# Kernel tuning notes

Hardware: AMD Instinct MI355X
Metric: run time of the kernel (lower is better)

Reference implementation:

```python
import jax, jax.numpy as jnp
import numpy as np

B, T, E, H, D = 2, 2048, 1024, 16, 64
SCALE = 1.0 / float(np.sqrt(D))


def setup_inputs() -> dict:
    key = jax.random.key(0)
    ks = jax.random.split(key, 8)
    n = lambda k, sh, s=1.0: jax.random.normal(k, sh, dtype=jnp.float32) * s
    # torch nn.Linear weights are [out_features, in_features]; xavier-ish scale
    return {
        "query": n(ks[0], (B, T, E)),
        "key_": n(ks[1], (B, T, E)),
        "value": n(ks[2], (B, T, E)),
        "attn_mask": n(ks[3], (T, T), 0.1),
        "Wq": n(ks[4], (H * D, E), 1.0 / float(np.sqrt(E))),
        "Wk": n(ks[5], (H * D, E), 1.0 / float(np.sqrt(E))),
        "Wv": n(ks[6], (H * D, E), 1.0 / float(np.sqrt(E))),
        "Wo": n(ks[7], (E, H * D), 1.0 / float(np.sqrt(H * D))),
    }


def reference(query, key_, value, attn_mask, Wq, Wk, Wv, Wo):
    # projections (no bias), reshape to [B, T, H, D]
    Q = (query @ Wq.T).reshape(B, T, H, D)
    K = (key_ @ Wk.T).reshape(B, -1, H, D)
    V = (value @ Wv.T).reshape(B, -1, H, D)
    # scores [B, T, H, S]; additive [T, S] mask broadcast over B and H
    score = jnp.einsum("bthd,bshd->bths", Q, K) * SCALE
    score = score + attn_mask[:, None, :]
    prob = jax.nn.softmax(score, axis=-1)  # dropout is identity in eval mode
    attn = jnp.einsum("bths,bshd->bthd", prob, V)  # [B, T, H, D]
    x = attn.reshape(B, T, H * D) @ Wo.T  # output projection
    return x
```

## Files before the change

kernel.cpp:

```cpp
#include <hip/hip_runtime.h>


typedef __attribute__((ext_vector_type(8))) short s8v;
typedef __attribute__((ext_vector_type(4))) float f4v;

typedef __attribute__((address_space(1))) const void* gas_t;
typedef __attribute__((address_space(3))) void* las_t;

#define GLOAD_LDS(src, dst) \
  __builtin_amdgcn_global_load_lds((gas_t)(src), (las_t)(dst), 16, 0, 0)
#define MFMA16(a, b, c) __builtin_amdgcn_mfma_f32_16x16x32_bf16((a), (b), (c), 0, 0, 0)

#if __has_builtin(__builtin_amdgcn_exp2f)
#define EXP2(x) __builtin_amdgcn_exp2f(x)
#else
#define EXP2(x) exp2f(x)
#endif

static constexpr int Bn = 2, Tn = 2048, En = 1024, Hn = 16, Dn = 64;
static constexpr float kScale = 0.125f;
static constexpr float kLog2e = 1.4426950408889634f;

union P8 { s8v v; unsigned short u[8]; };

__device__ __forceinline__ unsigned short f2bf(float f) {
  unsigned int x = __float_as_uint(f);
  x += 0x7fffu + ((x >> 16) & 1u);
  return (unsigned short)(x >> 16);
}

__device__ __forceinline__ int cvtpk(float lo, float hi) {
  int r;
  asm("v_cvt_pk_bf16_f32 %0, %1, %2" : "=v"(r) : "v"(lo), "v"(hi));
  return r;
}

__device__ __forceinline__ void cast8(const float* __restrict__ src, int j,
                                      unsigned short* __restrict__ out, int i) {
  float4 a = ((const float4*)src)[2 * j];
  float4 b = ((const float4*)src)[2 * j + 1];
  P8 p;
  p.u[0] = f2bf(a.x); p.u[1] = f2bf(a.y); p.u[2] = f2bf(a.z); p.u[3] = f2bf(a.w);
  p.u[4] = f2bf(b.x); p.u[5] = f2bf(b.y); p.u[6] = f2bf(b.z); p.u[7] = f2bf(b.w);
  ((s8v*)out)[i] = p.v;
}

__global__ void cast3_kernel(const float* __restrict__ a, const float* __restrict__ b,
                             const float* __restrict__ c,
                             unsigned short* __restrict__ out, int n8) {
  int i = blockIdx.x * blockDim.x + threadIdx.x;
  const int stride = gridDim.x * blockDim.x;
  const int total = 3 * n8;
  for (; i < total; i += stride) {
    const float* src = (i < n8) ? a : (i < 2 * n8) ? b : c;
    const int j = (i < n8) ? i : (i < 2 * n8) ? i - n8 : i - 2 * n8;
    cast8(src, j, out, i);
  }
}

__global__ void cast4_kernel(const float* __restrict__ a, const float* __restrict__ b,
                             const float* __restrict__ c, const float* __restrict__ d,
                             unsigned short* __restrict__ out, int n8) {
  int i = blockIdx.x * blockDim.x + threadIdx.x;
  const int stride = gridDim.x * blockDim.x;
  const int total = 4 * n8;
  for (; i < total; i += stride) {
    const int which = i / n8;
    const float* src = (which == 0) ? a : (which == 1) ? b : (which == 2) ? c : d;
    cast8(src, i - which * n8, out, i);
  }
}

__global__ __launch_bounds__(64) void maskpack_kernel(const float* __restrict__ mask,
                                                      unsigned int* __restrict__ mPB) {
  __shared__ float tile[16][65];
  const int qt = blockIdx.x, st = blockIdx.y;
  const int tid = threadIdx.x;
#pragma unroll
  for (int i = 0; i < 16; ++i)
    tile[i][tid] = mask[(size_t)(qt * 16 + i) * Tn + st * 64 + tid];
  __syncthreads();
  const int lr = tid & 15, lg = tid >> 4;
  float o[16];
#pragma unroll
  for (int n = 0; n < 4; ++n)
#pragma unroll
    for (int rg = 0; rg < 4; ++rg)
      o[n * 4 + rg] = tile[lr][n * 16 + lg * 4 + rg] * kLog2e;
  unsigned int wds[8];
#pragma unroll
  for (int i = 0; i < 8; ++i)
    wds[i] = ((unsigned int)f2bf(o[2 * i + 1]) << 16) | f2bf(o[2 * i]);
  uint4* dst = (uint4*)(mPB + ((size_t)(qt * 32 + st) * 64 + tid) * 8);
  dst[0] = make_uint4(wds[0], wds[1], wds[2], wds[3]);
  dst[1] = make_uint4(wds[4], wds[5], wds[6], wds[7]);
}

__global__ __launch_bounds__(256) void gemm3_kernel(
    const unsigned short* __restrict__ qx, const unsigned short* __restrict__ kx,
    const unsigned short* __restrict__ vxa, const unsigned short* __restrict__ wqx,
    const unsigned short* __restrict__ wkx, const unsigned short* __restrict__ wvx,
    unsigned short* __restrict__ Qh, unsigned short* __restrict__ Kh,
    unsigned short* __restrict__ Vtg) {
  constexpr int K = 1024;
  __shared__ unsigned short As[128 * 64];
  __shared__ unsigned short Bs[128 * 64];
  const int tid = threadIdx.x;
  const int w = tid >> 6, l = tid & 63;
  const int wr = w >> 1, wc = w & 1;
  const int lr = l & 15, lg = l >> 4;

  const int id0 = blockIdx.x;
  const int rid = (id0 & 7) * 96 + (id0 >> 3);
  const int z = rid >> 8;
  const int t8 = rid & 255;
  const int m0 = (z < 2) ? (t8 >> 3) * 128 : (t8 & 7) * 128;
  const int n0 = (z < 2) ? (t8 & 7) * 128 : (t8 >> 3) * 128;

  const unsigned short* A = (z == 0) ? qx : (z == 1) ? kx : wvx;
  const unsigned short* W = (z == 0) ? wqx : (z == 1) ? wkx : vxa;

  f4v acc[4][4] = {};

  for (int k0 = 0; k0 < K; k0 += 64) {
#pragma unroll
    for (int jj = 0; jj < 4; ++jj) {
      const int q = jj * 256 + tid;
      const int r = q >> 3, c = q & 7;
      const int cs = c ^ (r & 7);
      GLOAD_LDS(A + (size_t)(m0 + r) * K + k0 + cs * 8,
                (char*)As + (jj * 256 + w * 64) * 16);
      GLOAD_LDS(W + (size_t)(n0 + r) * K + k0 + cs * 8,
                (char*)Bs + (jj * 256 + w * 64) * 16);
    }
    __syncthreads();
#pragma unroll
    for (int kk = 0; kk < 2; ++kk) {
      s8v af[4], bf[4];
      const int kc = kk * 4 + lg;
#pragma unroll
      for (int i = 0; i < 4; ++i) {
        const int ra = wr * 64 + i * 16 + lr;
        const int rb = wc * 64 + i * 16 + lr;
        af[i] = *(const s8v*)((const char*)As + ra * 128 + ((kc ^ (ra & 7)) << 4));
        bf[i] = *(const s8v*)((const char*)Bs + rb * 128 + ((kc ^ (rb & 7)) << 4));
      }
#pragma unroll
      for (int mi = 0; mi < 4; ++mi)
#pragma unroll
        for (int nj = 0; nj < 4; ++nj)
          acc[mi][nj] = MFMA16(af[mi], bf[nj], acc[mi][nj]);
    }
    __syncthreads();
  }

  const float scale = (z == 0) ? kScale * kLog2e : 1.0f;
#pragma unroll
  for (int mi = 0; mi < 4; ++mi)
#pragma unroll
    for (int nj = 0; nj < 4; ++nj)
#pragma unroll
      for (int rg = 0; rg < 4; ++rg) {
        const int row = m0 + wr * 64 + mi * 16 + lg * 4 + rg;
        const int col = n0 + wc * 64 + nj * 16 + lr;
        const float v = acc[mi][nj][rg];
        if (z < 2) {
          const int b = row >> 11, t = row & (Tn - 1);
          const int hh = col >> 6, d = col & 63;
          unsigned short* o = (z == 0) ? Qh : Kh;
          o[(((size_t)(b * Hn + hh) * Tn + t) << 6) + d] = f2bf(v * scale);
        } else {
          const int hh = row >> 6, d = row & 63;
          const int b = col >> 11, t = col & (Tn - 1);
          Vtg[((size_t)(b * Hn + hh) * 64 + d) * Tn + t] = f2bf(v);
        }
      }
}

__global__ __launch_bounds__(256) void gemm_out(const unsigned short* __restrict__ A,
                                                const unsigned short* __restrict__ W,
                                                float* __restrict__ Cout) {
  constexpr int N = 1024, K = 1024;
  __shared__ unsigned short As[2][128 * 64];
  __shared__ unsigned short Bs[2][128 * 64];
  const int tid = threadIdx.x;
  const int w = tid >> 6, l = tid & 63;
  const int wr = w >> 1, wc = w & 1;
  const int lr = l & 15, lg = l >> 4;

  const int gx = gridDim.x;
  int id = blockIdx.y * gx + blockIdx.x;
  id = (id & 7) * 32 + (id >> 3);
  const int m0 = (id / gx) * 128, n0 = (id % gx) * 128;

  auto stage = [&](int k0, int buf) {
#pragma unroll
    for (int jj = 0; jj < 4; ++jj) {
      const int q = jj * 256 + tid;
      const int r = q >> 3, c = q & 7;
      const int cs = c ^ (r & 7);
      GLOAD_LDS(A + (size_t)(m0 + r) * K + k0 + cs * 8,
                (char*)As[buf] + (jj * 256 + w * 64) * 16);
      GLOAD_LDS(W + (size_t)(n0 + r) * K + k0 + cs * 8,
                (char*)Bs[buf] + (jj * 256 + w * 64) * 16);
    }
  };

  stage(0, 0);
  __syncthreads();

  f4v acc[4][4] = {};

  for (int k0 = 0, t = 0; k0 < K; k0 += 64, ++t) {
    const int cur = t & 1;
    if (k0 + 64 < K) stage(k0 + 64, cur ^ 1);
#pragma unroll
    for (int kk = 0; kk < 2; ++kk) {
      s8v af[4], bf[4];
      const int kc = kk * 4 + lg;
#pragma unroll
      for (int i = 0; i < 4; ++i) {
        const int ra = wr * 64 + i * 16 + lr;
        const int rb = wc * 64 + i * 16 + lr;
        af[i] = *(const s8v*)((const char*)As[cur] + ra * 128 + ((kc ^ (ra & 7)) << 4));
        bf[i] = *(const s8v*)((const char*)Bs[cur] + rb * 128 + ((kc ^ (rb & 7)) << 4));
      }
#pragma unroll
      for (int mi = 0; mi < 4; ++mi)
#pragma unroll
        for (int nj = 0; nj < 4; ++nj)
          acc[mi][nj] = MFMA16(af[mi], bf[nj], acc[mi][nj]);
    }
    __syncthreads();
  }

#pragma unroll
  for (int mi = 0; mi < 4; ++mi)
#pragma unroll
    for (int nj = 0; nj < 4; ++nj)
#pragma unroll
      for (int rg = 0; rg < 4; ++rg) {
        const int row = m0 + wr * 64 + mi * 16 + lg * 4 + rg;
        const int col = n0 + wc * 64 + nj * 16 + lr;
        Cout[(size_t)row * N + col] = acc[mi][nj][rg];
      }
}

__global__ __launch_bounds__(256, 4) void attn_kernel(
    const unsigned short* __restrict__ Q,
    const unsigned short* __restrict__ Kg,
    const unsigned short* __restrict__ Vt,
    const unsigned int* __restrict__ mPB,
    unsigned short* __restrict__ Out) {
  __shared__ unsigned short Ks[2][64 * 64];
  __shared__ unsigned short Vs[2][64 * 64];

  const int tid = threadIdx.x;
  const int w = tid >> 6, lane = tid & 63;
  const int lr = lane & 15, lg = lane >> 4;

  const int lin = blockIdx.x;
  const int xcd = lin & 7, slot = lin >> 3;
  const int bh = xcd * 4 + (slot >> 5);
  const int qtB = slot & 31;
  const int b = bh >> 4, h = bh & 15;

  const size_t hoff = (size_t)bh * Tn * Dn;
  const unsigned short* Qh = Q + hoff;
  const unsigned short* Kh = Kg + hoff;
  const unsigned short* Vh = Vt + hoff;
  const int qw = qtB * 64 + w * 16;
  const unsigned int* mp = mPB + ((size_t)(qtB * 4 + w) * 32 * 64 + lane) * 8;

  auto stage = [&](int s0, int buf) {
#pragma unroll
    for (int jj = 0; jj < 2; ++jj) {
      const int cq = jj * 256 + tid;
      const int r = cq >> 3, cc = cq & 7;
      const int cs = cc ^ (r & 7);
      GLOAD_LDS(Kh + (size_t)(s0 + r) * 64 + cs * 8,
                (char*)Ks[buf] + (jj * 256 + w * 64) * 16);
      GLOAD_LDS(Vh + (size_t)r * Tn + s0 + cs * 8,
                (char*)Vs[buf] + (jj * 256 + w * 64) * 16);
    }
  };

  s8v qf[2];
#pragma unroll
  for (int kk = 0; kk < 2; ++kk)
    qf[kk] = *(const s8v*)(Qh + (size_t)(qw + lr) * 64 + kk * 32 + lg * 8);

  float lsum = 0.f;
  f4v oacc[4] = {};

  const int srcA = lr + ((lg & 1) << 5);
  const int srcB = srcA + 16;
  const int hi = lg >> 1;

  stage(0, 0);
  __syncthreads();

  for (int s0 = 0, t = 0; s0 < Tn; s0 += 64, ++t, mp += 512) {
    const int cur = t & 1;
    if (s0 + 64 < Tn) stage(s0 + 64, cur ^ 1);

    const uint4 u0 = *(const uint4*)(mp);
    const uint4 u1 = *(const uint4*)(mp + 4);
    const unsigned int wd[8] = {u0.x, u0.y, u0.z, u0.w, u1.x, u1.y, u1.z, u1.w};
    f4v scT[4];
#pragma unroll
    for (int n = 0; n < 4; ++n) {
      scT[n][0] = __uint_as_float(wd[2 * n] << 16);
      scT[n][1] = __uint_as_float(wd[2 * n] & 0xffff0000u);
      scT[n][2] = __uint_as_float(wd[2 * n + 1] << 16);
      scT[n][3] = __uint_as_float(wd[2 * n + 1] & 0xffff0000u);
    }

#pragma unroll
    for (int kk = 0; kk < 2; ++kk)
#pragma unroll
      for (int n = 0; n < 4; ++n) {
        const int row = n * 16 + lr;
        s8v kf = *(const s8v*)((const char*)Ks[cur] + row * 128 +
                               (((kk * 4 + lg) ^ (lr & 7)) << 4));
        scT[n] = MFMA16(kf, qf[kk], scT[n]);
      }

    float ssum = 0.f;
#pragma unroll
    for (int n = 0; n < 4; ++n)
#pragma unroll
      for (int rg = 0; rg < 4; ++rg) {
        const float p = EXP2(scT[n][rg]);
        scT[n][rg] = p;
        ssum += p;
      }
    ssum += __shfl_xor(ssum, 16);
    ssum += __shfl_xor(ssum, 32);
    lsum += ssum;

    int pw0[4], pw1[4];
#pragma unroll
    for (int n = 0; n < 4; ++n) {
      pw0[n] = cvtpk(scT[n][0], scT[n][1]);
      pw1[n] = cvtpk(scT[n][2], scT[n][3]);
    }

#pragma unroll
    for (int kk = 0; kk < 2; ++kk) {
      const int a0 = __shfl(pw0[2 * kk], srcA), b0 = __shfl(pw0[2 * kk + 1], srcA);
      const int a1 = __shfl(pw1[2 * kk], srcA), b1 = __shfl(pw1[2 * kk + 1], srcA);
      const int a2 = __shfl(pw0[2 * kk], srcB), b2 = __shfl(pw0[2 * kk + 1], srcB);
      const int a3 = __shfl(pw1[2 * kk], srcB), b3 = __shfl(pw1[2 * kk + 1], srcB);
      union { s8v v; int x[4]; } pf;
      pf.x[0] = hi ? b0 : a0;
      pf.x[1] = hi ? b1 : a1;
      pf.x[2] = hi ? b2 : a2;
      pf.x[3] = hi ? b3 : a3;
#pragma unroll
      for (int n = 0; n < 4; ++n) {
        const int rd = n * 16 + lr;
        s8v vf = *(const s8v*)((const char*)Vs[cur] + rd * 128 +
                               (((kk * 4 + lg) ^ (lr & 7)) << 4));
        oacc[n] = MFMA16(pf.v, vf, oacc[n]);
      }
    }
    __syncthreads();
  }

#pragma unroll
  for (int rg = 0; rg < 4; ++rg) {
    const float inv = 1.f / __shfl(lsum, lg * 4 + rg);
    const int t = qw + lg * 4 + rg;
#pragma unroll
    for (int n = 0; n < 4; ++n) {
      const int d = n * 16 + lr;
      Out[((size_t)(b * Tn + t) * Hn + h) * 64 + d] = f2bf(oacc[n][rg] * inv);
    }
  }
}

extern "C" void kernel_launch(void* const* d_in, const int* in_sizes, int n_in,
                              void* d_out, int out_size, void* d_ws, size_t ws_size,
                              hipStream_t stream) {
  (void)in_sizes; (void)n_in; (void)out_size; (void)ws_size;
  const float* query = (const float*)d_in[0];
  const float* key_  = (const float*)d_in[1];
  const float* value = (const float*)d_in[2];
  const float* mask  = (const float*)d_in[3];
  const float* Wq    = (const float*)d_in[4];
  const float* Wk    = (const float*)d_in[5];
  const float* Wv    = (const float*)d_in[6];
  const float* Wo    = (const float*)d_in[7];
  float* out = (float*)d_out;

  char* ws = (char*)d_ws;
  const size_t MB = 1024 * 1024;
  unsigned short* qx  = (unsigned short*)(ws + 0 * MB);
  unsigned short* kx  = (unsigned short*)(ws + 8 * MB);
  unsigned short* vx  = (unsigned short*)(ws + 16 * MB);
  unsigned short* Qh  = (unsigned short*)(ws + 24 * MB);
  unsigned short* Kh  = (unsigned short*)(ws + 32 * MB);
  unsigned short* Vtg = (unsigned short*)(ws + 40 * MB);
  unsigned short* atb = (unsigned short*)(ws + 48 * MB);
  unsigned short* wqx = (unsigned short*)(ws + 56 * MB);
  unsigned short* wkx = (unsigned short*)(ws + 58 * MB);
  unsigned short* wvx = (unsigned short*)(ws + 60 * MB);
  unsigned short* wox = (unsigned short*)(ws + 62 * MB);
  unsigned int* mPB = (unsigned int*)(ws + 0 * MB);

  const int nBig = Bn * Tn * En / 8;
  const int nW   = En * En / 8;
  cast3_kernel<<<2048, 256, 0, stream>>>(query, key_, value, qx, nBig);
  cast4_kernel<<<1024, 256, 0, stream>>>(Wq, Wk, Wv, Wo, wqx, nW);

  gemm3_kernel<<<768, 256, 0, stream>>>(qx, kx, vx, wqx, wkx, wvx, Qh, Kh, Vtg);

  maskpack_kernel<<<dim3(128, 32), 64, 0, stream>>>(mask, mPB);

  attn_kernel<<<1024, 256, 0, stream>>>(Qh, Kh, Vtg, mPB, atb);

  gemm_out<<<dim3(8, 32), 256, 0, stream>>>(atb, wox, out);
}
```

Before: 160.2 us.

## Process two query sub-tiles per wave in attention to reuse K/V fragments

The attention kernel now runs 2 waves per block instead of 4, and each wave handles two 16-row query tiles. K and V fragments are loaded from LDS once per step into registers and reused for both tiles, which halves LDS reads per query row. The staging loop is widened so fewer threads fill the same tiles. The cost is higher register pressure (two accumulator sets plus cached K/V fragments) and fewer waves per block, which may reduce latency hiding.

```diff
diff --git a/kernel.cpp b/kernel.cpp
--- a/kernel.cpp
+++ b/kernel.cpp
@@ -246,7 +246,7 @@
       }
 }
 
-__global__ __launch_bounds__(256, 4) void attn_kernel(
+__global__ __launch_bounds__(128, 2) void attn_kernel(
     const unsigned short* __restrict__ Q,
     const unsigned short* __restrict__ Kg,
     const unsigned short* __restrict__ Vt,
@@ -269,29 +269,32 @@
   const unsigned short* Qh = Q + hoff;
   const unsigned short* Kh = Kg + hoff;
   const unsigned short* Vh = Vt + hoff;
-  const int qw = qtB * 64 + w * 16;
-  const unsigned int* mp = mPB + ((size_t)(qtB * 4 + w) * 32 * 64 + lane) * 8;
+  const int qwA = qtB * 64 + w * 32;
+  const int qwB = qwA + 16;
+  const unsigned int* mp = mPB + ((size_t)(qtB * 4 + w * 2) * 2048 + lane) * 8;
 
   auto stage = [&](int s0, int buf) {
 #pragma unroll
-    for (int jj = 0; jj < 2; ++jj) {
-      const int cq = jj * 256 + tid;
+    for (int jj = 0; jj < 4; ++jj) {
+      const int cq = jj * 128 + tid;
       const int r = cq >> 3, cc = cq & 7;
       const int cs = cc ^ (r & 7);
       GLOAD_LDS(Kh + (size_t)(s0 + r) * 64 + cs * 8,
-                (char*)Ks[buf] + (jj * 256 + w * 64) * 16);
+                (char*)Ks[buf] + (jj * 128 + w * 64) * 16);
       GLOAD_LDS(Vh + (size_t)r * Tn + s0 + cs * 8,
-                (char*)Vs[buf] + (jj * 256 + w * 64) * 16);
+                (char*)Vs[buf] + (jj * 128 + w * 64) * 16);
     }
   };
 
-  s8v qf[2];
-#pragma unroll
-  for (int kk = 0; kk < 2; ++kk)
-    qf[kk] = *(const s8v*)(Qh + (size_t)(qw + lr) * 64 + kk * 32 + lg * 8);
-
-  float lsum = 0.f;
-  f4v oacc[4] = {};
+  s8v qfA[2], qfB[2];
+#pragma unroll
+  for (int kk = 0; kk < 2; ++kk) {
+    qfA[kk] = *(const s8v*)(Qh + (size_t)(qwA + lr) * 64 + kk * 32 + lg * 8);
+    qfB[kk] = *(const s8v*)(Qh + (size_t)(qwB + lr) * 64 + kk * 32 + lg * 8);
+  }
+
+  float lsumA = 0.f, lsumB = 0.f;
+  f4v oaccA[4] = {}, oaccB[4] = {};
 
   const int srcA = lr + ((lg & 1) << 5);
   const int srcB = srcA + 16;
@@ -304,78 +307,135 @@
     const int cur = t & 1;
     if (s0 + 64 < Tn) stage(s0 + 64, cur ^ 1);
 
-    const uint4 u0 = *(const uint4*)(mp);
-    const uint4 u1 = *(const uint4*)(mp + 4);
-    const unsigned int wd[8] = {u0.x, u0.y, u0.z, u0.w, u1.x, u1.y, u1.z, u1.w};
-    f4v scT[4];
-#pragma unroll
-    for (int n = 0; n < 4; ++n) {
-      scT[n][0] = __uint_as_float(wd[2 * n] << 16);
-      scT[n][1] = __uint_as_float(wd[2 * n] & 0xffff0000u);
-      scT[n][2] = __uint_as_float(wd[2 * n + 1] << 16);
-      scT[n][3] = __uint_as_float(wd[2 * n + 1] & 0xffff0000u);
-    }
-
+    s8v kf[2][4], vf[2][4];
 #pragma unroll
     for (int kk = 0; kk < 2; ++kk)
 #pragma unroll
       for (int n = 0; n < 4; ++n) {
         const int row = n * 16 + lr;
-        s8v kf = *(const s8v*)((const char*)Ks[cur] + row * 128 +
-                               (((kk * 4 + lg) ^ (lr & 7)) << 4));
-        scT[n] = MFMA16(kf, qf[kk], scT[n]);
-      }
-
-    float ssum = 0.f;
-#pragma unroll
-    for (int n = 0; n < 4; ++n)
-#pragma unroll
-      for (int rg = 0; rg < 4; ++rg) {
-        const float p = EXP2(scT[n][rg]);
-        scT[n][rg] = p;
-        ssum += p;
-      }
-    ssum += __shfl_xor(ssum, 16);
-    ssum += __shfl_xor(ssum, 32);
-    lsum += ssum;
-
-    int pw0[4], pw1[4];
-#pragma unroll
-    for (int n = 0; n < 4; ++n) {
-      pw0[n] = cvtpk(scT[n][0], scT[n][1]);
-      pw1[n] = cvtpk(scT[n][2], scT[n][3]);
-    }
-
-#pragma unroll
-    for (int kk = 0; kk < 2; ++kk) {
-      const int a0 = __shfl(pw0[2 * kk], srcA), b0 = __shfl(pw0[2 * kk + 1], srcA);
-      const int a1 = __shfl(pw1[2 * kk], srcA), b1 = __shfl(pw1[2 * kk + 1], srcA);
-      const int a2 = __shfl(pw0[2 * kk], srcB), b2 = __shfl(pw0[2 * kk + 1], srcB);
-      const int a3 = __shfl(pw1[2 * kk], srcB), b3 = __shfl(pw1[2 * kk + 1], srcB);
-      union { s8v v; int x[4]; } pf;
-      pf.x[0] = hi ? b0 : a0;
-      pf.x[1] = hi ? b1 : a1;
-      pf.x[2] = hi ? b2 : a2;
-      pf.x[3] = hi ? b3 : a3;
+        const int coff = ((kk * 4 + lg) ^ (lr & 7)) << 4;
+        kf[kk][n] = *(const s8v*)((const char*)Ks[cur] + row * 128 + coff);
+        vf[kk][n] = *(const s8v*)((const char*)Vs[cur] + row * 128 + coff);
+      }
+
+    {
+      const uint4 u0 = *(const uint4*)(mp);
+      const uint4 u1 = *(const uint4*)(mp + 4);
+      const unsigned int wd[8] = {u0.x, u0.y, u0.z, u0.w, u1.x, u1.y, u1.z, u1.w};
+      f4v scT[4];
 #pragma unroll
       for (int n = 0; n < 4; ++n) {
-        const int rd = n * 16 + lr;
-        s8v vf = *(const s8v*)((const char*)Vs[cur] + rd * 128 +
-                               (((kk * 4 + lg) ^ (lr & 7)) << 4));
-        oacc[n] = MFMA16(pf.v, vf, oacc[n]);
-      }
-    }
+        scT[n][0] = __uint_as_float(wd[2 * n] << 16);
+        scT[n][1] = __uint_as_float(wd[2 * n] & 0xffff0000u);
+        scT[n][2] = __uint_as_float(wd[2 * n + 1] << 16);
+        scT[n][3] = __uint_as_float(wd[2 * n + 1] & 0xffff0000u);
+      }
+#pragma unroll
+      for (int kk = 0; kk < 2; ++kk)
+#pragma unroll
+        for (int n = 0; n < 4; ++n)
+          scT[n] = MFMA16(kf[kk][n], qfA[kk], scT[n]);
+      float ssum = 0.f;
+#pragma unroll
+      for (int n = 0; n < 4; ++n)
+#pragma unroll
+        for (int rg = 0; rg < 4; ++rg) {
+          const float p = EXP2(scT[n][rg]);
+          scT[n][rg] = p;
+          ssum += p;
+        }
+      ssum += __shfl_xor(ssum, 16);
+      ssum += __shfl_xor(ssum, 32);
+      lsumA += ssum;
+      int pw0[4], pw1[4];
+#pragma unroll
+      for (int n = 0; n < 4; ++n) {
+        pw0[n] = cvtpk(scT[n][0], scT[n][1]);
+        pw1[n] = cvtpk(scT[n][2], scT[n][3]);
+      }
+#pragma unroll
+      for (int kk = 0; kk < 2; ++kk) {
+        const int a0 = __shfl(pw0[2 * kk], srcA), b0 = __shfl(pw0[2 * kk + 1], srcA);
+        const int a1 = __shfl(pw1[2 * kk], srcA), b1 = __shfl(pw1[2 * kk + 1], srcA);
+        const int a2 = __shfl(pw0[2 * kk], srcB), b2 = __shfl(pw0[2 * kk + 1], srcB);
+        const int a3 = __shfl(pw1[2 * kk], srcB), b3 = __shfl(pw1[2 * kk + 1], srcB);
+        union { s8v v; int x[4]; } pf;
+        pf.x[0] = hi ? b0 : a0;
+        pf.x[1] = hi ? b1 : a1;
+        pf.x[2] = hi ? b2 : a2;
+        pf.x[3] = hi ? b3 : a3;
+#pragma unroll
+        for (int n = 0; n < 4; ++n)
+          oaccA[n] = MFMA16(pf.v, vf[kk][n], oaccA[n]);
+      }
+    }
+
+    {
+      const uint4 u0 = *(const uint4*)(mp + 16384);
+      const uint4 u1 = *(const uint4*)(mp + 16388);
+      const unsigned int wd[8] = {u0.x, u0.y, u0.z, u0.w, u1.x, u1.y, u1.z, u1.w};
+      f4v scT[4];
+#pragma unroll
+      for (int n = 0; n < 4; ++n) {
+        scT[n][0] = __uint_as_float(wd[2 * n] << 16);
+        scT[n][1] = __uint_as_float(wd[2 * n] & 0xffff0000u);
+        scT[n][2] = __uint_as_float(wd[2 * n + 1] << 16);
+        scT[n][3] = __uint_as_float(wd[2 * n + 1] & 0xffff0000u);
+      }
+#pragma unroll
+      for (int kk = 0; kk < 2; ++kk)
+#pragma unroll
+        for (int n = 0; n < 4; ++n)
+          scT[n] = MFMA16(kf[kk][n], qfB[kk], scT[n]);
+      float ssum = 0.f;
+#pragma unroll
+      for (int n = 0; n < 4; ++n)
+#pragma unroll
+        for (int rg = 0; rg < 4; ++rg) {
+          const float p = EXP2(scT[n][rg]);
+          scT[n][rg] = p;
+          ssum += p;
+        }
+      ssum += __shfl_xor(ssum, 16);
+      ssum += __shfl_xor(ssum, 32);
+      lsumB += ssum;
+      int pw0[4], pw1[4];
+#pragma unroll
+      for (int n = 0; n < 4; ++n) {
+        pw0[n] = cvtpk(scT[n][0], scT[n][1]);
+        pw1[n] = cvtpk(scT[n][2], scT[n][3]);
+      }
+#pragma unroll
+      for (int kk = 0; kk < 2; ++kk) {
+        const int a0 = __shfl(pw0[2 * kk], srcA), b0 = __shfl(pw0[2 * kk + 1], srcA);
+        const int a1 = __shfl(pw1[2 * kk], srcA), b1 = __shfl(pw1[2 * kk + 1], srcA);
+        const int a2 = __shfl(pw0[2 * kk], srcB), b2 = __shfl(pw0[2 * kk + 1], srcB);
+        const int a3 = __shfl(pw1[2 * kk], srcB), b3 = __shfl(pw1[2 * kk + 1], srcB);
+        union { s8v v; int x[4]; } pf;
+        pf.x[0] = hi ? b0 : a0;
+        pf.x[1] = hi ? b1 : a1;
+        pf.x[2] = hi ? b2 : a2;
+        pf.x[3] = hi ? b3 : a3;
+#pragma unroll
+        for (int n = 0; n < 4; ++n)
+          oaccB[n] = MFMA16(pf.v, vf[kk][n], oaccB[n]);
+      }
+    }
+
     __syncthreads();
   }
 
 #pragma unroll
   for (int rg = 0; rg < 4; ++rg) {
-    const float inv = 1.f / __shfl(lsum, lg * 4 + rg);
-    const int t = qw + lg * 4 + rg;
+    const float invA = 1.f / __shfl(lsumA, lg * 4 + rg);
+    const float invB = 1.f / __shfl(lsumB, lg * 4 + rg);
+    const int tA = qwA + lg * 4 + rg;
+    const int tB = qwB + lg * 4 + rg;
 #pragma unroll
     for (int n = 0; n < 4; ++n) {
       const int d = n * 16 + lr;
-      Out[((size_t)(b * Tn + t) * Hn + h) * 64 + d] = f2bf(oacc[n][rg] * inv);
+      Out[((size_t)(b * Tn + tA) * Hn + h) * 64 + d] = f2bf(oaccA[n][rg] * invA);
+      Out[((size_t)(b * Tn + tB) * Hn + h) * 64 + d] = f2bf(oaccB[n][rg] * invB);
     }
   }
 }
@@ -418,7 +478,7 @@
 
   maskpack_kernel<<<dim3(128, 32), 64, 0, stream>>>(mask, mPB);
 
-  attn_kernel<<<1024, 256, 0, stream>>>(Qh, Kh, Vtg, mPB, atb);
+  attn_kernel<<<1024, 128, 0, stream>>>(Qh, Kh, Vtg, mPB, atb);
 
   gemm_out<<<dim3(8, 32), 256, 0, stream>>>(atb, wox, out);
 }
```

Result: slower. 166.2 us (+3.8%).

## Split attention key range into two halves and add combine kernel

Applied to the files above, without the earlier changes.

Each attention block now processes only half of the key sequence, so the grid doubles to 2048 blocks. Each block writes unnormalized fp16 partial outputs and row sums to workspace. A new combine kernel adds the two partials, normalizes, and writes the bf16 attention output. This aims to raise parallelism and latency hiding in the attention stage. In exchange it adds an extra kernel launch, extra global traffic for the partials, and a risk of fp16 overflow in the unnormalized sums.

```diff
diff --git a/kernel.cpp b/kernel.cpp
--- a/kernel.cpp
+++ b/kernel.cpp
@@ -27,6 +27,12 @@
   unsigned int x = __float_as_uint(f);
   x += 0x7fffu + ((x >> 16) & 1u);
   return (unsigned short)(x >> 16);
+}
+
+__device__ __forceinline__ unsigned short f2h(float f) {
+  union { _Float16 h; unsigned short u; } c;
+  c.h = (_Float16)f;
+  return c.u;
 }
 
 __device__ __forceinline__ int cvtpk(float lo, float hi) {
@@ -251,7 +257,8 @@
     const unsigned short* __restrict__ Kg,
     const unsigned short* __restrict__ Vt,
     const unsigned int* __restrict__ mPB,
-    unsigned short* __restrict__ Out) {
+    unsigned short* __restrict__ oP0, unsigned short* __restrict__ oP1,
+    float* __restrict__ ls0, float* __restrict__ ls1) {
   __shared__ unsigned short Ks[2][64 * 64];
   __shared__ unsigned short Vs[2][64 * 64];
 
@@ -261,7 +268,8 @@
 
   const int lin = blockIdx.x;
   const int xcd = lin & 7, slot = lin >> 3;
-  const int bh = xcd * 4 + (slot >> 5);
+  const int bh = xcd * 4 + (slot >> 6);
+  const int half = (slot >> 5) & 1;
   const int qtB = slot & 31;
   const int b = bh >> 4, h = bh & 15;
 
@@ -270,7 +278,12 @@
   const unsigned short* Kh = Kg + hoff;
   const unsigned short* Vh = Vt + hoff;
   const int qw = qtB * 64 + w * 16;
-  const unsigned int* mp = mPB + ((size_t)(qtB * 4 + w) * 32 * 64 + lane) * 8;
+  const unsigned int* mp =
+      mPB + ((size_t)(qtB * 4 + w) * 2048 + lane) * 8 + half * 8192;
+  const int sBeg = half * 1024, sEnd = sBeg + 1024;
+
+  unsigned short* oph = half ? oP1 : oP0;
+  float* lsh = half ? ls1 : ls0;
 
   auto stage = [&](int s0, int buf) {
 #pragma unroll
@@ -297,12 +310,12 @@
   const int srcB = srcA + 16;
   const int hi = lg >> 1;
 
-  stage(0, 0);
+  stage(sBeg, 0);
   __syncthreads();
 
-  for (int s0 = 0, t = 0; s0 < Tn; s0 += 64, ++t, mp += 512) {
+  for (int s0 = sBeg, t = 0; s0 < sEnd; s0 += 64, ++t, mp += 512) {
     const int cur = t & 1;
-    if (s0 + 64 < Tn) stage(s0 + 64, cur ^ 1);
+    if (s0 + 64 < sEnd) stage(s0 + 64, cur ^ 1);
 
     const uint4 u0 = *(const uint4*)(mp);
     const uint4 u1 = *(const uint4*)(mp + 4);
@@ -370,14 +383,34 @@
 
 #pragma unroll
   for (int rg = 0; rg < 4; ++rg) {
-    const float inv = 1.f / __shfl(lsum, lg * 4 + rg);
     const int t = qw + lg * 4 + rg;
 #pragma unroll
     for (int n = 0; n < 4; ++n) {
       const int d = n * 16 + lr;
-      Out[((size_t)(b * Tn + t) * Hn + h) * 64 + d] = f2bf(oacc[n][rg] * inv);
-    }
-  }
+      oph[((size_t)(b * Tn + t) * Hn + h) * 64 + d] = f2h(oacc[n][rg]);
+    }
+  }
+  if (lg == 0) {
+    lsh[(size_t)(b * Tn + qw + lr) * Hn + h] = lsum;
+  }
+}
+
+__global__ __launch_bounds__(256) void combine_kernel(
+    const unsigned short* __restrict__ oP0, const unsigned short* __restrict__ oP1,
+    const float* __restrict__ ls0, const float* __restrict__ ls1,
+    unsigned short* __restrict__ atb) {
+  const int idx = blockIdx.x * 256 + threadIdx.x;
+  const int row = idx >> 3;
+  const size_t base = (size_t)idx * 8;
+  union H8 { s8v v; _Float16 h[8]; } a, c;
+  a.v = *(const s8v*)(oP0 + base);
+  c.v = *(const s8v*)(oP1 + base);
+  const float inv = 1.f / (ls0[row] + ls1[row]);
+  P8 p;
+#pragma unroll
+  for (int j = 0; j < 8; ++j)
+    p.u[j] = f2bf(((float)a.h[j] + (float)c.h[j]) * inv);
+  *(s8v*)(atb + base) = p.v;
 }
 
 extern "C" void kernel_launch(void* const* d_in, const int* in_sizes, int n_in,
@@ -402,12 +435,16 @@
   unsigned short* Qh  = (unsigned short*)(ws + 24 * MB);
   unsigned short* Kh  = (unsigned short*)(ws + 32 * MB);
   unsigned short* Vtg = (unsigned short*)(ws + 40 * MB);
-  unsigned short* atb = (unsigned short*)(ws + 48 * MB);
+  unsigned short* oP1 = (unsigned short*)(ws + 48 * MB);
   unsigned short* wqx = (unsigned short*)(ws + 56 * MB);
   unsigned short* wkx = (unsigned short*)(ws + 58 * MB);
   unsigned short* wvx = (unsigned short*)(ws + 60 * MB);
   unsigned short* wox = (unsigned short*)(ws + 62 * MB);
-  unsigned int* mPB = (unsigned int*)(ws + 0 * MB);
+  unsigned int*   mPB = (unsigned int*)(ws + 0 * MB);
+  unsigned short* oP0 = (unsigned short*)(ws + 9 * MB);
+  float* ls0 = (float*)(ws + 17 * MB);
+  float* ls1 = (float*)(ws + 17 * MB + 256 * 1024);
+  unsigned short* atb = Qh;
 
   const int nBig = Bn * Tn * En / 8;
   const int nW   = En * En / 8;
@@ -418,7 +455,9 @@
 
   maskpack_kernel<<<dim3(128, 32), 64, 0, stream>>>(mask, mPB);
 
-  attn_kernel<<<1024, 256, 0, stream>>>(Qh, Kh, Vtg, mPB, atb);
+  attn_kernel<<<2048, 256, 0, stream>>>(Qh, Kh, Vtg, mPB, oP0, oP1, ls0, ls1);
+
+  combine_kernel<<<2048, 256, 0, stream>>>(oP0, oP1, ls0, ls1, atb);
 
   gemm_out<<<dim3(8, 32), 256, 0, stream>>>(atb, wox, out);
 }
```

Result: slower. 166.4 us (+3.9%).

## Fuse fp32-to-bf16 input casts into QKV projection GEMM staging

Applied to the files above, without the earlier changes.

Removes the separate cast kernels for query/key/value and Wq/Wk/Wv. The QKV GEMM now loads fp32 directly, converts to bf16 in registers and writes to swizzled LDS. Only Wo still gets a standalone cast. This drops a full read-write pass over the activations and weights. In exchange, the GEMM loses its async global_load_lds path and reads twice the bytes per tile, with the conversion on the critical path before each barrier.

```diff
diff --git a/kernel.cpp b/kernel.cpp
--- a/kernel.cpp
+++ b/kernel.cpp
@@ -35,39 +35,17 @@
   return r;
 }
 
-__device__ __forceinline__ void cast8(const float* __restrict__ src, int j,
-                                      unsigned short* __restrict__ out, int i) {
-  float4 a = ((const float4*)src)[2 * j];
-  float4 b = ((const float4*)src)[2 * j + 1];
-  P8 p;
-  p.u[0] = f2bf(a.x); p.u[1] = f2bf(a.y); p.u[2] = f2bf(a.z); p.u[3] = f2bf(a.w);
-  p.u[4] = f2bf(b.x); p.u[5] = f2bf(b.y); p.u[6] = f2bf(b.z); p.u[7] = f2bf(b.w);
-  ((s8v*)out)[i] = p.v;
-}
-
-__global__ void cast3_kernel(const float* __restrict__ a, const float* __restrict__ b,
-                             const float* __restrict__ c,
+__global__ void cast1_kernel(const float* __restrict__ in,
                              unsigned short* __restrict__ out, int n8) {
   int i = blockIdx.x * blockDim.x + threadIdx.x;
   const int stride = gridDim.x * blockDim.x;
-  const int total = 3 * n8;
-  for (; i < total; i += stride) {
-    const float* src = (i < n8) ? a : (i < 2 * n8) ? b : c;
-    const int j = (i < n8) ? i : (i < 2 * n8) ? i - n8 : i - 2 * n8;
-    cast8(src, j, out, i);
-  }
-}
-
-__global__ void cast4_kernel(const float* __restrict__ a, const float* __restrict__ b,
-                             const float* __restrict__ c, const float* __restrict__ d,
-                             unsigned short* __restrict__ out, int n8) {
-  int i = blockIdx.x * blockDim.x + threadIdx.x;
-  const int stride = gridDim.x * blockDim.x;
-  const int total = 4 * n8;
-  for (; i < total; i += stride) {
-    const int which = i / n8;
-    const float* src = (which == 0) ? a : (which == 1) ? b : (which == 2) ? c : d;
-    cast8(src, i - which * n8, out, i);
+  for (; i < n8; i += stride) {
+    float4 a = ((const float4*)in)[2 * i];
+    float4 b = ((const float4*)in)[2 * i + 1];
+    P8 p;
+    p.u[0] = f2bf(a.x); p.u[1] = f2bf(a.y); p.u[2] = f2bf(a.z); p.u[3] = f2bf(a.w);
+    p.u[4] = f2bf(b.x); p.u[5] = f2bf(b.y); p.u[6] = f2bf(b.z); p.u[7] = f2bf(b.w);
+    ((s8v*)out)[i] = p.v;
   }
 }
 
@@ -97,9 +75,9 @@
 }
 
 __global__ __launch_bounds__(256) void gemm3_kernel(
-    const unsigned short* __restrict__ qx, const unsigned short* __restrict__ kx,
-    const unsigned short* __restrict__ vxa, const unsigned short* __restrict__ wqx,
-    const unsigned short* __restrict__ wkx, const unsigned short* __restrict__ wvx,
+    const float* __restrict__ query, const float* __restrict__ key_,
+    const float* __restrict__ value, const float* __restrict__ Wq,
+    const float* __restrict__ Wk, const float* __restrict__ Wv,
     unsigned short* __restrict__ Qh, unsigned short* __restrict__ Kh,
     unsigned short* __restrict__ Vtg) {
   constexpr int K = 1024;
@@ -117,22 +95,31 @@
   const int m0 = (z < 2) ? (t8 >> 3) * 128 : (t8 & 7) * 128;
   const int n0 = (z < 2) ? (t8 & 7) * 128 : (t8 >> 3) * 128;
 
-  const unsigned short* A = (z == 0) ? qx : (z == 1) ? kx : wvx;
-  const unsigned short* W = (z == 0) ? wqx : (z == 1) ? wkx : vxa;
-
-  f4v acc[4][4] = {};
-
-  for (int k0 = 0; k0 < K; k0 += 64) {
+  const float* A = (z == 0) ? query : (z == 1) ? key_ : Wv;
+  const float* W = (z == 0) ? Wq : (z == 1) ? Wk : value;
+
+  auto stage = [&](const float* src, int baseRow, int k0, unsigned short* lds) {
 #pragma unroll
     for (int jj = 0; jj < 4; ++jj) {
       const int q = jj * 256 + tid;
       const int r = q >> 3, c = q & 7;
-      const int cs = c ^ (r & 7);
-      GLOAD_LDS(A + (size_t)(m0 + r) * K + k0 + cs * 8,
-                (char*)As + (jj * 256 + w * 64) * 16);
-      GLOAD_LDS(W + (size_t)(n0 + r) * K + k0 + cs * 8,
-                (char*)Bs + (jj * 256 + w * 64) * 16);
-    }
+      const float4* g =
+          (const float4*)(src + (size_t)(baseRow + r) * K + k0 + c * 8);
+      const float4 a = g[0], b4 = g[1];
+      union { int x[4]; s8v v; } pk;
+      pk.x[0] = cvtpk(a.x, a.y);
+      pk.x[1] = cvtpk(a.z, a.w);
+      pk.x[2] = cvtpk(b4.x, b4.y);
+      pk.x[3] = cvtpk(b4.z, b4.w);
+      *(s8v*)((char*)lds + ((q & ~7) + (c ^ (r & 7))) * 16) = pk.v;
+    }
+  };
+
+  f4v acc[4][4] = {};
+
+  for (int k0 = 0; k0 < K; k0 += 64) {
+    stage(A, m0, k0, As);
+    stage(W, n0, k0, Bs);
     __syncthreads();
 #pragma unroll
     for (int kk = 0; kk < 2; ++kk) {
@@ -270,7 +257,7 @@
   const unsigned short* Kh = Kg + hoff;
   const unsigned short* Vh = Vt + hoff;
   const int qw = qtB * 64 + w * 16;
-  const unsigned int* mp = mPB + ((size_t)(qtB * 4 + w) * 32 * 64 + lane) * 8;
+  const unsigned int* mp = mPB + ((size_t)(qtB * 4 + w) * 2048 + lane) * 8;
 
   auto stage = [&](int s0, int buf) {
 #pragma unroll
@@ -396,27 +383,19 @@
 
   char* ws = (char*)d_ws;
   const size_t MB = 1024 * 1024;
-  unsigned short* qx  = (unsigned short*)(ws + 0 * MB);
-  unsigned short* kx  = (unsigned short*)(ws + 8 * MB);
-  unsigned short* vx  = (unsigned short*)(ws + 16 * MB);
+  unsigned int*   mPB = (unsigned int*)(ws + 0 * MB);
   unsigned short* Qh  = (unsigned short*)(ws + 24 * MB);
   unsigned short* Kh  = (unsigned short*)(ws + 32 * MB);
   unsigned short* Vtg = (unsigned short*)(ws + 40 * MB);
   unsigned short* atb = (unsigned short*)(ws + 48 * MB);
-  unsigned short* wqx = (unsigned short*)(ws + 56 * MB);
-  unsigned short* wkx = (unsigned short*)(ws + 58 * MB);
-  unsigned short* wvx = (unsigned short*)(ws + 60 * MB);
   unsigned short* wox = (unsigned short*)(ws + 62 * MB);
-  unsigned int* mPB = (unsigned int*)(ws + 0 * MB);
-
-  const int nBig = Bn * Tn * En / 8;
-  const int nW   = En * En / 8;
-  cast3_kernel<<<2048, 256, 0, stream>>>(query, key_, value, qx, nBig);
-  cast4_kernel<<<1024, 256, 0, stream>>>(Wq, Wk, Wv, Wo, wqx, nW);
-
-  gemm3_kernel<<<768, 256, 0, stream>>>(qx, kx, vx, wqx, wkx, wvx, Qh, Kh, Vtg);
-
+
+  const int nW = En * En / 8;
   maskpack_kernel<<<dim3(128, 32), 64, 0, stream>>>(mask, mPB);
+  cast1_kernel<<<512, 256, 0, stream>>>(Wo, wox, nW);
+
+  gemm3_kernel<<<768, 256, 0, stream>>>(query, key_, value, Wq, Wk, Wv,
+                                        Qh, Kh, Vtg);
 
   attn_kernel<<<1024, 256, 0, stream>>>(Qh, Kh, Vtg, mPB, atb);
 
```

Measured after the change: 168.4 us. +5.1%, slower.
